# Kernel optimization log

Hardware: AMD Instinct MI355X
Metric: run time of the kernel (lower is better)

The kernel has to match this reference:

```python
import jax, jax.numpy as jnp
import numpy as np

WIDTHS = [16384, 4096, 1024, 16]
LATENT = WIDTHS[-1]

# static polynomial-library index sets (poly_order = 3)
_PAIRS = np.array([(i, j) for i in range(LATENT) for j in range(i, LATENT)]).T
_TRIPS = np.array([(i, j, k) for i in range(LATENT) for j in range(i, LATENT) for k in range(j, LATENT)]).T


def sindy_library(z):
    # [1]*d ++ z ++ upper-tri pairwise products ++ upper-tri triple products -> [984]
    ones = jnp.ones((LATENT,), dtype=z.dtype)
    quad = z[_PAIRS[0]] * z[_PAIRS[1]]
    cub = z[_TRIPS[0]] * z[_TRIPS[1]] * z[_TRIPS[2]]
    return jnp.concatenate([ones, z, quad, cub])


def setup_inputs() -> dict:
    key = jax.random.key(0)
    ks = jax.random.split(key, 32)
    d = {
        'x': jax.random.normal(ks[0], (WIDTHS[0],), dtype=jnp.float32),
        'dx': jax.random.normal(ks[1], (WIDTHS[0],), dtype=jnp.float32),
        'ddx': jax.random.normal(ks[2], (WIDTHS[0],), dtype=jnp.float32),
    }
    ki = 3
    # encoder Linear(widths[i], widths[i+1]); xavier-ish scale
    for i in range(len(WIDTHS) - 1):
        fin, fout = WIDTHS[i], WIDTHS[i + 1]
        s = jnp.sqrt(2.0 / (fin + fout)).astype(jnp.float32)
        d[f'we_w{i}'] = jax.random.normal(ks[ki], (fout, fin), dtype=jnp.float32) * s; ki += 1
        d[f'we_b{i}'] = jax.random.normal(ks[ki], (fout,), dtype=jnp.float32) * 0.01; ki += 1
    # decoder Linear(widths[-i-1], widths[-i-2])
    for i in range(len(WIDTHS) - 1):
        fin, fout = WIDTHS[-i - 1], WIDTHS[-i - 2]
        s = jnp.sqrt(2.0 / (fin + fout)).astype(jnp.float32)
        d[f'wd_w{i}'] = jax.random.normal(ks[ki], (fout, fin), dtype=jnp.float32) * s; ki += 1
        d[f'wd_b{i}'] = jax.random.normal(ks[ki], (fout,), dtype=jnp.float32) * 0.01; ki += 1
    sindy_dim = 2 * LATENT + _PAIRS.shape[1] + _TRIPS.shape[1]  # 984
    d['E_w'] = jnp.ones((LATENT, sindy_dim), dtype=jnp.float32)  # nn.init.ones_
    d['E_b'] = jnp.zeros((LATENT,), dtype=jnp.float32)
    return d


def reference(x, dx, ddx,
              we_w0, we_b0, we_w1, we_b1, we_w2, we_b2,
              wd_w0, wd_b0, wd_w1, wd_b1, wd_w2, wd_b2,
              E_w, E_b):
    def enc(v):
        h = jax.nn.sigmoid(we_w0 @ v + we_b0)
        h = jax.nn.sigmoid(we_w1 @ h + we_b1)
        return we_w2 @ h + we_b2  # identity on last layer

    def dec(v):
        h = jax.nn.sigmoid(wd_w0 @ v + wd_b0)
        h = jax.nn.sigmoid(wd_w1 @ h + wd_b1)
        return wd_w2 @ h + wd_b2

    z = enc(x)                                   # [latent]
    gx_enc = jax.jacrev(enc)(x)                  # [latent, input_dim]
    dz = gx_enc @ dx                             # [latent]
    theta = sindy_library(z)                     # [sindy_dim]
    dzb = E_w @ theta + E_b                      # [latent]
    xb = dec(z)                                  # [input_dim]
    gx_dec = jax.jacfwd(dec)(z)                  # [input_dim, latent]
    dxb = gx_dec @ dzb                           # [input_dim]
    return (z, dz, dzb, xb, dxb)
```

## Files before the change

### kernel.cpp

```cpp
#include <hip/hip_runtime.h>
#include <math.h>

template <bool SIG>
__global__ __launch_bounds__(256) void dual_matvec(
    const float* __restrict__ W, const float* __restrict__ b,
    const float* __restrict__ v, const float* __restrict__ t,
    float* __restrict__ h_out, float* __restrict__ t_out, int ncols)
{
    const int row = blockIdx.x;
    const int tid = threadIdx.x;
    const float4* __restrict__ W4 = (const float4*)(W + (size_t)row * ncols);
    const float4* __restrict__ v4 = (const float4*)v;
    const float4* __restrict__ t4 = (const float4*)t;
    const int nvec = ncols >> 2;

    float ah = 0.f, at = 0.f;
    for (int i = tid; i < nvec; i += 256) {
        float4 w = W4[i];
        float4 a = v4[i];
        float4 c = t4[i];
        ah += w.x * a.x + w.y * a.y + w.z * a.z + w.w * a.w;
        at += w.x * c.x + w.y * c.y + w.z * c.z + w.w * c.w;
    }
    #pragma unroll
    for (int off = 32; off > 0; off >>= 1) {
        ah += __shfl_down(ah, off, 64);
        at += __shfl_down(at, off, 64);
    }
    __shared__ float sh[4], st[4];
    const int wave = tid >> 6;
    if ((tid & 63) == 0) { sh[wave] = ah; st[wave] = at; }
    __syncthreads();
    if (tid == 0) {
        float hsum = sh[0] + sh[1] + sh[2] + sh[3];
        float tsum = st[0] + st[1] + st[2] + st[3];
        hsum += b[row];
        if (SIG) {
            float s = 1.f / (1.f + expf(-hsum));
            h_out[row] = s;
            t_out[row] = s * (1.f - s) * tsum;
        } else {
            h_out[row] = hsum;
            t_out[row] = tsum;
        }
    }
}

__global__ __launch_bounds__(256) void head_kernel(
    const float* __restrict__ W2, const float* __restrict__ b2,
    const float* __restrict__ h2, const float* __restrict__ t2,
    const float* __restrict__ Ew, const float* __restrict__ Eb,
    const float* __restrict__ U0, const float* __restrict__ c0,
    float* __restrict__ out,
    float* __restrict__ g1, float* __restrict__ s1)
{
    __shared__ float z_s[16], dz_s[16], dzb_s[16];
    __shared__ float theta[984];
    __shared__ float red_h[256], red_t[256];

    const int tid = threadIdx.x;
    const int r = tid >> 4;
    const int c = tid & 15;

    {
        const float* Wr = W2 + r * 1024;
        float ah = 0.f, at = 0.f;
        for (int idx = c; idx < 1024; idx += 16) {
            float w = Wr[idx];
            ah += w * h2[idx];
            at += w * t2[idx];
        }
        red_h[tid] = ah; red_t[tid] = at;
        __syncthreads();
        if (c == 0) {
            float zs = 0.f, ts = 0.f;
            for (int j = 0; j < 16; j++) { zs += red_h[(r << 4) + j]; ts += red_t[(r << 4) + j]; }
            z_s[r] = zs + b2[r];
            dz_s[r] = ts;
        }
        __syncthreads();
    }

    if (tid < 16) { theta[tid] = 1.0f; theta[16 + tid] = z_s[tid]; }
    for (int t = tid; t < 136; t += 256) {
        int rem = t, i = 0;
        while (rem >= 16 - i) { rem -= 16 - i; i++; }
        int j = i + rem;
        theta[32 + t] = z_s[i] * z_s[j];
    }
    for (int t = tid; t < 816; t += 256) {
        int rem = t, i = 0;
        for (;;) { int cnt = (16 - i) * (17 - i) >> 1; if (rem < cnt) break; rem -= cnt; i++; }
        int j = i;
        while (rem >= 16 - j) { rem -= 16 - j; j++; }
        int k = j + rem;
        theta[168 + t] = z_s[i] * z_s[j] * z_s[k];
    }
    __syncthreads();

    {
        const float* Er = Ew + r * 984;
        float a = 0.f;
        for (int idx = c; idx < 984; idx += 16) a += Er[idx] * theta[idx];
        red_h[tid] = a;
        __syncthreads();
        if (c == 0) {
            float s = 0.f;
            for (int j = 0; j < 16; j++) s += red_h[(r << 4) + j];
            dzb_s[r] = s + Eb[r];
        }
        __syncthreads();
    }

    if (tid < 16) {
        out[tid]      = z_s[tid];
        out[16 + tid] = dz_s[tid];
        out[32 + tid] = dzb_s[tid];
    }

    for (int row = tid; row < 1024; row += 256) {
        const float* Ur = U0 + row * 16;
        float ah = 0.f, at = 0.f;
        #pragma unroll
        for (int k = 0; k < 16; k++) {
            float w = Ur[k];
            ah += w * z_s[k];
            at += w * dzb_s[k];
        }
        ah += c0[row];
        float s = 1.f / (1.f + expf(-ah));
        g1[row] = s;
        s1[row] = s * (1.f - s) * at;
    }
}

extern "C" void kernel_launch(void* const* d_in, const int* in_sizes, int n_in,
                              void* d_out, int out_size, void* d_ws, size_t ws_size,
                              hipStream_t stream)
{
    const float* x     = (const float*)d_in[0];
    const float* dx    = (const float*)d_in[1];
    const float* we_w0 = (const float*)d_in[3];
    const float* we_b0 = (const float*)d_in[4];
    const float* we_w1 = (const float*)d_in[5];
    const float* we_b1 = (const float*)d_in[6];
    const float* we_w2 = (const float*)d_in[7];
    const float* we_b2 = (const float*)d_in[8];
    const float* wd_w0 = (const float*)d_in[9];
    const float* wd_b0 = (const float*)d_in[10];
    const float* wd_w1 = (const float*)d_in[11];
    const float* wd_b1 = (const float*)d_in[12];
    const float* wd_w2 = (const float*)d_in[13];
    const float* wd_b2 = (const float*)d_in[14];
    const float* E_w   = (const float*)d_in[15];
    const float* E_b   = (const float*)d_in[16];

    float* out = (float*)d_out;
    float* ws  = (float*)d_ws;

    float* h1 = ws;
    float* t1 = ws + 4096;
    float* h2 = ws + 8192;
    float* t2 = ws + 9216;
    float* g1 = ws + 10240;
    float* s1 = ws + 11264;
    float* g2 = ws + 12288;
    float* s2 = ws + 16384;

    float* xb  = out + 48;
    float* dxb = out + 48 + 16384;

    dual_matvec<true><<<4096, 256, 0, stream>>>(we_w0, we_b0, x, dx, h1, t1, 16384);
    dual_matvec<true><<<1024, 256, 0, stream>>>(we_w1, we_b1, h1, t1, h2, t2, 4096);
    head_kernel<<<1, 256, 0, stream>>>(we_w2, we_b2, h2, t2, E_w, E_b,
                                       wd_w0, wd_b0, out, g1, s1);
    dual_matvec<true><<<4096, 256, 0, stream>>>(wd_w1, wd_b1, g1, s1, g2, s2, 1024);
    dual_matvec<false><<<16384, 256, 0, stream>>>(wd_w2, wd_b2, g2, s2, xb, dxb, 4096);
}
```

Before: 622.6 us.

## Switch GEMVs to one-row-per-wave with compile-time widths and nontemporal loads

After: 551.9 us. -11.4%, faster.

```diff
diff --git a/kernel.cpp b/kernel.cpp
--- a/kernel.cpp
+++ b/kernel.cpp
@@ -1,52 +1,54 @@
 #include <hip/hip_runtime.h>
 #include <math.h>
 
-template <bool SIG>
-__global__ __launch_bounds__(256) void dual_matvec(
+typedef float vfloat4 __attribute__((ext_vector_type(4)));
+
+template <int NCOLS, bool SIG>
+__global__ __launch_bounds__(256) void gemv_dual(
     const float* __restrict__ W, const float* __restrict__ b,
     const float* __restrict__ v, const float* __restrict__ t,
-    float* __restrict__ h_out, float* __restrict__ t_out, int ncols)
+    float* __restrict__ h_out, float* __restrict__ t_out, int nrows)
 {
-    const int row = blockIdx.x;
-    const int tid = threadIdx.x;
-    const float4* __restrict__ W4 = (const float4*)(W + (size_t)row * ncols);
-    const float4* __restrict__ v4 = (const float4*)v;
-    const float4* __restrict__ t4 = (const float4*)t;
-    const int nvec = ncols >> 2;
+    constexpr int NV = NCOLS / 4;
+    constexpr int ITER = NV / 64;
+    const int lane = threadIdx.x & 63;
+    const int wave = (int)((blockIdx.x * blockDim.x + threadIdx.x) >> 6);
+    const int nw = (int)((gridDim.x * blockDim.x) >> 6);
+    const vfloat4* __restrict__ v4 = (const vfloat4*)v;
+    const vfloat4* __restrict__ t4 = (const vfloat4*)t;
 
-    float ah = 0.f, at = 0.f;
-    for (int i = tid; i < nvec; i += 256) {
-        float4 w = W4[i];
-        float4 a = v4[i];
-        float4 c = t4[i];
-        ah += w.x * a.x + w.y * a.y + w.z * a.z + w.w * a.w;
-        at += w.x * c.x + w.y * c.y + w.z * c.z + w.w * c.w;
-    }
-    #pragma unroll
-    for (int off = 32; off > 0; off >>= 1) {
-        ah += __shfl_down(ah, off, 64);
-        at += __shfl_down(at, off, 64);
-    }
-    __shared__ float sh[4], st[4];
-    const int wave = tid >> 6;
-    if ((tid & 63) == 0) { sh[wave] = ah; st[wave] = at; }
-    __syncthreads();
-    if (tid == 0) {
-        float hsum = sh[0] + sh[1] + sh[2] + sh[3];
-        float tsum = st[0] + st[1] + st[2] + st[3];
-        hsum += b[row];
-        if (SIG) {
-            float s = 1.f / (1.f + expf(-hsum));
-            h_out[row] = s;
-            t_out[row] = s * (1.f - s) * tsum;
-        } else {
-            h_out[row] = hsum;
-            t_out[row] = tsum;
+    for (int row = wave; row < nrows; row += nw) {
+        const vfloat4* __restrict__ W4 = (const vfloat4*)(W + (size_t)row * NCOLS);
+        float ah = 0.f, at = 0.f;
+        #pragma unroll 4
+        for (int k = 0; k < ITER; ++k) {
+            const int i = lane + 64 * k;
+            vfloat4 w = __builtin_nontemporal_load(&W4[i]);
+            vfloat4 a = v4[i];
+            vfloat4 c = t4[i];
+            ah += w.x * a.x + w.y * a.y + w.z * a.z + w.w * a.w;
+            at += w.x * c.x + w.y * c.y + w.z * c.z + w.w * c.w;
+        }
+        #pragma unroll
+        for (int off = 32; off; off >>= 1) {
+            ah += __shfl_down(ah, off, 64);
+            at += __shfl_down(at, off, 64);
+        }
+        if (lane == 0) {
+            ah += b[row];
+            if (SIG) {
+                float s = 1.f / (1.f + expf(-ah));
+                h_out[row] = s;
+                t_out[row] = s * (1.f - s) * at;
+            } else {
+                h_out[row] = ah;
+                t_out[row] = at;
+            }
         }
     }
 }
 
-__global__ __launch_bounds__(256) void head_kernel(
+__global__ __launch_bounds__(1024) void head_kernel(
     const float* __restrict__ W2, const float* __restrict__ b2,
     const float* __restrict__ h2, const float* __restrict__ t2,
     const float* __restrict__ Ew, const float* __restrict__ Eb,
@@ -56,61 +58,66 @@
 {
     __shared__ float z_s[16], dz_s[16], dzb_s[16];
     __shared__ float theta[984];
-    __shared__ float red_h[256], red_t[256];
 
     const int tid = threadIdx.x;
-    const int r = tid >> 4;
-    const int c = tid & 15;
+    const int lane = tid & 63;
+    const int r = tid >> 6;
 
     {
-        const float* Wr = W2 + r * 1024;
+        const vfloat4* Wr = (const vfloat4*)(W2 + r * 1024);
+        const vfloat4* h4 = (const vfloat4*)h2;
+        const vfloat4* t4 = (const vfloat4*)t2;
         float ah = 0.f, at = 0.f;
-        for (int idx = c; idx < 1024; idx += 16) {
-            float w = Wr[idx];
-            ah += w * h2[idx];
-            at += w * t2[idx];
+        #pragma unroll
+        for (int k = 0; k < 4; ++k) {
+            const int i = lane + 64 * k;
+            vfloat4 w = Wr[i];
+            vfloat4 a = h4[i];
+            vfloat4 c = t4[i];
+            ah += w.x * a.x + w.y * a.y + w.z * a.z + w.w * a.w;
+            at += w.x * c.x + w.y * c.y + w.z * c.z + w.w * c.w;
         }
-        red_h[tid] = ah; red_t[tid] = at;
-        __syncthreads();
-        if (c == 0) {
-            float zs = 0.f, ts = 0.f;
-            for (int j = 0; j < 16; j++) { zs += red_h[(r << 4) + j]; ts += red_t[(r << 4) + j]; }
-            z_s[r] = zs + b2[r];
-            dz_s[r] = ts;
+        #pragma unroll
+        for (int off = 32; off; off >>= 1) {
+            ah += __shfl_down(ah, off, 64);
+            at += __shfl_down(at, off, 64);
         }
-        __syncthreads();
+        if (lane == 0) {
+            z_s[r] = ah + b2[r];
+            dz_s[r] = at;
+        }
     }
+    __syncthreads();
 
     if (tid < 16) { theta[tid] = 1.0f; theta[16 + tid] = z_s[tid]; }
-    for (int t = tid; t < 136; t += 256) {
+    for (int t = tid; t < 136; t += 1024) {
         int rem = t, i = 0;
         while (rem >= 16 - i) { rem -= 16 - i; i++; }
-        int j = i + rem;
-        theta[32 + t] = z_s[i] * z_s[j];
+        theta[32 + t] = z_s[i] * z_s[i + rem];
     }
-    for (int t = tid; t < 816; t += 256) {
+    for (int t = tid; t < 816; t += 1024) {
         int rem = t, i = 0;
         for (;;) { int cnt = (16 - i) * (17 - i) >> 1; if (rem < cnt) break; rem -= cnt; i++; }
         int j = i;
         while (rem >= 16 - j) { rem -= 16 - j; j++; }
-        int k = j + rem;
-        theta[168 + t] = z_s[i] * z_s[j] * z_s[k];
+        theta[168 + t] = z_s[i] * z_s[j] * z_s[j + rem];
     }
     __syncthreads();
 
     {
-        const float* Er = Ew + r * 984;
+        const vfloat4* Er = (const vfloat4*)(Ew + r * 984);
+        const vfloat4* th4 = (const vfloat4*)theta;
         float a = 0.f;
-        for (int idx = c; idx < 984; idx += 16) a += Er[idx] * theta[idx];
-        red_h[tid] = a;
-        __syncthreads();
-        if (c == 0) {
-            float s = 0.f;
-            for (int j = 0; j < 16; j++) s += red_h[(r << 4) + j];
-            dzb_s[r] = s + Eb[r];
+        for (int i = lane; i < 246; i += 64) {
+            vfloat4 w = Er[i];
+            vfloat4 x = th4[i];
+            a += w.x * x.x + w.y * x.y + w.z * x.z + w.w * x.w;
         }
-        __syncthreads();
+        #pragma unroll
+        for (int off = 32; off; off >>= 1) a += __shfl_down(a, off, 64);
+        if (lane == 0) dzb_s[r] = a + Eb[r];
     }
+    __syncthreads();
 
     if (tid < 16) {
         out[tid]      = z_s[tid];
@@ -118,19 +125,19 @@
         out[32 + tid] = dzb_s[tid];
     }
 
-    for (int row = tid; row < 1024; row += 256) {
-        const float* Ur = U0 + row * 16;
+    {
+        const vfloat4* U4 = (const vfloat4*)(U0 + tid * 16);
         float ah = 0.f, at = 0.f;
         #pragma unroll
-        for (int k = 0; k < 16; k++) {
-            float w = Ur[k];
-            ah += w * z_s[k];
-            at += w * dzb_s[k];
+        for (int q = 0; q < 4; ++q) {
+            vfloat4 w = U4[q];
+            ah += w.x * z_s[4*q] + w.y * z_s[4*q+1] + w.z * z_s[4*q+2] + w.w * z_s[4*q+3];
+            at += w.x * dzb_s[4*q] + w.y * dzb_s[4*q+1] + w.z * dzb_s[4*q+2] + w.w * dzb_s[4*q+3];
         }
-        ah += c0[row];
+        ah += c0[tid];
         float s = 1.f / (1.f + expf(-ah));
-        g1[row] = s;
-        s1[row] = s * (1.f - s) * at;
+        g1[tid] = s;
+        s1[tid] = s * (1.f - s) * at;
     }
 }
 
@@ -170,10 +177,10 @@
     float* xb  = out + 48;
     float* dxb = out + 48 + 16384;
 
-    dual_matvec<true><<<4096, 256, 0, stream>>>(we_w0, we_b0, x, dx, h1, t1, 16384);
-    dual_matvec<true><<<1024, 256, 0, stream>>>(we_w1, we_b1, h1, t1, h2, t2, 4096);
-    head_kernel<<<1, 256, 0, stream>>>(we_w2, we_b2, h2, t2, E_w, E_b,
-                                       wd_w0, wd_b0, out, g1, s1);
-    dual_matvec<true><<<4096, 256, 0, stream>>>(wd_w1, wd_b1, g1, s1, g2, s2, 1024);
-    dual_matvec<false><<<16384, 256, 0, stream>>>(wd_w2, wd_b2, g2, s2, xb, dxb, 4096);
+    gemv_dual<16384, true><<<1024, 256, 0, stream>>>(we_w0, we_b0, x, dx, h1, t1, 4096);
+    gemv_dual<4096, true><<<256, 256, 0, stream>>>(we_w1, we_b1, h1, t1, h2, t2, 1024);
+    head_kernel<<<1, 1024, 0, stream>>>(we_w2, we_b2, h2, t2, E_w, E_b,
+                                        wd_w0, wd_b0, out, g1, s1);
+    gemv_dual<1024, true><<<1024, 256, 0, stream>>>(wd_w1, wd_b1, g1, s1, g2, s2, 4096);
+    gemv_dual<4096, false><<<4096, 256, 0, stream>>>(wd_w2, wd_b2, g2, s2, xb, dxb, 16384);
 }
```
